# Performance work log

Hardware: AMD Instinct MI355X
Metric: run time of the kernel (lower is better)

The kernel has to match this reference:

```python
import jax, jax.numpy as jnp
import numpy as np

EPS = 1e-8


def setup_inputs() -> dict:
    key = jax.random.key(0)
    ks = jax.random.split(key, 10)
    B, Cin, H, W = 16, 256, 64, 64
    D, C = 128, 32
    return {
        "f_curr": jax.random.normal(ks[0], (B, Cin, H, W), jnp.float32),
        "mu_prior": jax.random.normal(ks[1], (B, D, C), jnp.float32),
        "log_sigma_prior": jax.random.normal(ks[2], (B, D, C), jnp.float32),
        "pi_prior": jax.random.uniform(ks[3], (B, C), jnp.float32),
        "mu_post": jax.random.normal(ks[4], (B, D), jnp.float32),
        "log_sigma_post": jax.random.normal(ks[5], (B, D), jnp.float32),
        "noise_cluster": jax.random.normal(ks[6], (B, D), jnp.float32),
        "noise_z": jax.random.normal(ks[7], (B, D), jnp.float32),
        "proj_W": jax.random.normal(ks[8], (Cin, Cin + D), jnp.float32) * 0.02,
        "proj_b": jax.random.normal(ks[9], (Cin,), jnp.float32) * 0.02,
    }


def reference(f_curr, mu_prior, log_sigma_prior, pi_prior, mu_post,
              log_sigma_post, noise_cluster, noise_z, proj_W, proj_b):
    sg = jax.lax.stop_gradient

    # ---- _cluster_sampler (all stats detached in the original) ----
    mu_p, ls_p = sg(mu_post), sg(log_sigma_post)          # [B, D]
    mu_pr, ls_pr = sg(mu_prior), sg(log_sigma_prior)      # [B, D, C]
    z_post = mu_p + jnp.exp(ls_p) * noise_cluster          # Normal(mu, exp(ls)).sample()
    sigma_pr = jnp.exp(ls_pr)
    # Normal log_prob of z_post[:, :, None] under each cluster -> [B, D, C]
    log_probs = (-ls_pr - 0.5 * jnp.log(2.0 * jnp.pi)
                 - (z_post[:, :, None] - mu_pr) ** 2 / (2.0 * sigma_pr ** 2))
    log_prob_c = jnp.sum(log_probs, axis=1)                # [B, C]
    pi_post = jax.nn.softmax(log_prob_c, axis=1)           # [B, C]

    # ---- z_c = Normal(mu_post, exp(ls)+eps).sample()  (no grad: .sample()) ----
    z_c = sg(mu_post + (jnp.exp(log_sigma_post) + EPS) * noise_z)  # [B, D]

    # ---- _f_combine: concat + 1x1 conv, computed as split matmuls ----
    Cin = f_curr.shape[1]
    Wf, Wz = proj_W[:, :Cin], proj_W[:, Cin:]              # [Cin,Cin], [Cin,D]
    bias = jnp.einsum('bd,od->bo', z_c, Wz) + proj_b       # spatially-constant part
    f_out = jnp.einsum('bchw,oc->bohw', f_curr, Wf) + bias[:, :, None, None]

    # ---- _kld ----
    mu_post_e = mu_post[:, :, None]                        # [B, D, 1]
    ls_post_e = log_sigma_post[:, :, None]
    sigma_prior = jnp.exp(log_sigma_prior)
    sigma_post = jnp.exp(ls_post_e)
    kl_g = (log_sigma_prior - ls_post_e
            + (sigma_post ** 2 + (mu_post_e - mu_prior) ** 2)
            / (2.0 * sigma_prior ** 2 + EPS) - 0.5)
    kl_g = jnp.sum(kl_g, axis=1)                           # [B, C]
    kl_g_weighted = jnp.sum(pi_post * kl_g, axis=1)        # [B]
    kl_cat = jnp.sum(pi_post * (jnp.log(pi_post + EPS) - jnp.log(pi_prior + EPS)), axis=1)  # [B]
    kl_std = jnp.sum(-ls_post_e + 0.5 * (jnp.exp(2.0 * ls_post_e) + mu_post_e ** 2) - 0.5,
                     axis=1)                               # [B, 1]
    # NOTE: original torch code broadcasts [B] + [B,1] -> [B,B] before mean; replicated here.
    kld = jnp.mean((kl_g_weighted + kl_cat) + kl_std)

    return f_out, kld
```

## Files before the change

### kernel.cpp

```cpp
#include <hip/hip_runtime.h>
#include <math.h>

#define EPS_F 1e-8f

typedef __attribute__((ext_vector_type(8))) short bf16x8;
typedef __attribute__((ext_vector_type(4))) float f32x4;

__device__ inline short f2bf(float f) {
    union { float f; unsigned u; } v; v.f = f;
    unsigned r = (v.u + 0x7fffu + ((v.u >> 16) & 1u)) >> 16;
    return (short)r;
}

__global__ __launch_bounds__(256) void prelim_kernel(
    const float* __restrict__ mu_prior,
    const float* __restrict__ ls_prior,
    const float* __restrict__ pi_prior,
    const float* __restrict__ mu_post,
    const float* __restrict__ ls_post,
    const float* __restrict__ noise_c,
    const float* __restrict__ noise_z,
    const float* __restrict__ projW,
    const float* __restrict__ projb,
    float* __restrict__ ws_bias,
    short* __restrict__ ws_A,
    float* __restrict__ kld_out)
{
    const int b = blockIdx.x;
    const int t = threadIdx.x;

    {
        const float* wrow = projW + t * 384 + b * 16;
        bf16x8 w0, w1;
#pragma unroll
        for (int j = 0; j < 8; ++j) w0[j] = f2bf(wrow[j]);
#pragma unroll
        for (int j = 0; j < 8; ++j) w1[j] = f2bf(wrow[8 + j]);
        *(bf16x8*)&ws_A[(b * 2 + 0) * 2048 + t * 8] = w0;
        *(bf16x8*)&ws_A[(b * 2 + 1) * 2048 + t * 8] = w1;
    }

    __shared__ float s_zpost[128];
    __shared__ float s_zc[128];
    __shared__ float s_mu[128];
    __shared__ float s_e2[128];
    __shared__ float s_lsp[128];
    __shared__ float s_kstd[128];
    __shared__ float s_p1[8][32];
    __shared__ float s_p2[8][32];

    if (t < 128) {
        const float mu = mu_post[b * 128 + t];
        const float ls = ls_post[b * 128 + t];
        const float el = __expf(ls);
        s_zpost[t] = mu + el * noise_c[b * 128 + t];
        s_zc[t]    = mu + (el + EPS_F) * noise_z[b * 128 + t];
        s_mu[t]    = mu;
        s_e2[t]    = el * el;
        s_lsp[t]   = ls;
        s_kstd[t]  = -ls + 0.5f * (el * el + mu * mu) - 0.5f;
    }
    __syncthreads();

    {
        const int c = t & 31;
        const int g = t >> 5;
        const float* mpB = mu_prior + b * 4096;
        const float* lpB = ls_prior + b * 4096;
        float lp = 0.f, kg = 0.f;
#pragma unroll 4
        for (int j = 0; j < 16; ++j) {
            const int d = g * 16 + j;
            const float mpr  = mpB[d * 32 + c];
            const float lpr  = lpB[d * 32 + c];
            const float inv2 = 0.5f * __expf(-2.f * lpr);
            const float zd   = s_zpost[d] - mpr;
            lp += -lpr - 0.91893853320467274f - zd * zd * inv2;
            const float dm   = s_mu[d] - mpr;
            const float e2pr = __expf(2.f * lpr);
            kg += lpr - s_lsp[d]
                + (s_e2[d] + dm * dm) * __builtin_amdgcn_rcpf(2.f * e2pr + EPS_F)
                - 0.5f;
        }
        s_p1[g][c] = lp;
        s_p2[g][c] = kg;
    }
    __syncthreads();

    if (t < 64) {
        const int c = t & 31;
        float lp = 0.f, kg = 0.f;
#pragma unroll
        for (int g = 0; g < 8; ++g) { lp += s_p1[g][c]; kg += s_p2[g][c]; }
        float ks = s_kstd[c] + s_kstd[c + 32] + s_kstd[c + 64] + s_kstd[c + 96];
        const float pp = pi_prior[b * 32 + c];

        float m = lp;
#pragma unroll
        for (int o = 16; o; o >>= 1) m = fmaxf(m, __shfl_xor(m, o, 32));
        const float e = __expf(lp - m);
        float den = e;
#pragma unroll
        for (int o = 16; o; o >>= 1) den += __shfl_xor(den, o, 32);
        const float pi = e * __builtin_amdgcn_rcpf(den);
        float tot = pi * kg + pi * (__logf(pi + EPS_F) - __logf(pp + EPS_F));
#pragma unroll
        for (int o = 16; o; o >>= 1) tot += __shfl_xor(tot, o, 32);
#pragma unroll
        for (int o = 16; o; o >>= 1) ks += __shfl_xor(ks, o, 32);
        if (t == 0) atomicAdd(kld_out, (tot + ks) * 0.0625f);
    }

    {
        const int o = t;
        const float4* wrow = (const float4*)(projW + o * 384 + 256);
        float sum = projb[o];
#pragma unroll 8
        for (int j = 0; j < 32; ++j) {
            const float4 w = wrow[j];
            sum += s_zc[4 * j + 0] * w.x + s_zc[4 * j + 1] * w.y +
                   s_zc[4 * j + 2] * w.z + s_zc[4 * j + 3] * w.w;
        }
        ws_bias[b * 256 + o] = sum;
    }
}

__global__ __launch_bounds__(256) void gemm_kernel(
    const float* __restrict__ F,
    const short* __restrict__ wsA,
    const float* __restrict__ bias,
    float* __restrict__ O)
{
    const int nT = blockIdx.x;
    const int b  = blockIdx.y;

    __shared__ short Bl[32][64][8];
    __shared__ float s_bias[256];

    const int tid  = threadIdx.x;
    const int lane = tid & 63;
    const int wave = tid >> 6;
    const int kg   = lane >> 4;
    const int lm   = lane & 15;

    s_bias[tid] = bias[b * 256 + tid];

    const int sn4 = (tid & 15) * 4;
    const int skb = (tid >> 4) * 16;
    const float* fp = F + (size_t)b * 1048576 + (size_t)skb * 4096
                    + nT * 64 + sn4;

    float4 ld[16];
#pragma unroll
    for (int i = 0; i < 16; ++i)
        ld[i] = *(const float4*)(fp + (size_t)i * 4096);

#pragma unroll
    for (int h = 0; h < 2; ++h) {
        const int kgi = (skb >> 3) + h;
#pragma unroll
        for (int c = 0; c < 4; ++c) {
            bf16x8 v;
#pragma unroll
            for (int j = 0; j < 8; ++j) {
                const float4 q = ld[h * 8 + j];
                v[j] = f2bf(c == 0 ? q.x : c == 1 ? q.y : c == 2 ? q.z : q.w);
            }
            *(bf16x8*)&Bl[kgi][sn4 + c][0] = v;
        }
    }
    __syncthreads();

    const short* aBase = wsA + (size_t)kg * 2048 + (wave * 64 + lm) * 8;

    f32x4 acc[4][4];
#pragma unroll
    for (int i = 0; i < 4; ++i)
#pragma unroll
        for (int j = 0; j < 4; ++j) acc[i][j] = (f32x4){0.f, 0.f, 0.f, 0.f};

#pragma unroll
    for (int kc = 0; kc < 8; ++kc) {
        bf16x8 aF[4], bF[4];
#pragma unroll
        for (int mt = 0; mt < 4; ++mt)
            aF[mt] = *(const bf16x8*)(aBase + (size_t)kc * 8192 + mt * 128);
#pragma unroll
        for (int nt = 0; nt < 4; ++nt)
            bF[nt] = *(const bf16x8*)&Bl[kc * 4 + kg][nt * 16 + lm][0];

#pragma unroll
        for (int mt = 0; mt < 4; ++mt)
#pragma unroll
            for (int nt = 0; nt < 4; ++nt)
                acc[mt][nt] = __builtin_amdgcn_mfma_f32_16x16x32_bf16(
                    aF[mt], bF[nt], acc[mt][nt], 0, 0, 0);
    }

    float* Ob = O + (size_t)b * 1048576 + nT * 64;
    const int rbase = wave * 64 + kg * 4;
    const int cbase = lm;
#pragma unroll
    for (int mt = 0; mt < 4; ++mt) {
#pragma unroll
        for (int r = 0; r < 4; ++r) {
            const int row = rbase + mt * 16 + r;
            const float bb = s_bias[row];
            float* orow = Ob + (size_t)row * 4096 + cbase;
#pragma unroll
            for (int nt = 0; nt < 4; ++nt)
                orow[nt * 16] = acc[mt][nt][r] + bb;
        }
    }
}

extern "C" void kernel_launch(void* const* d_in, const int* in_sizes, int n_in,
                              void* d_out, int out_size, void* d_ws, size_t ws_size,
                              hipStream_t stream) {
    const float* f_curr   = (const float*)d_in[0];
    const float* mu_prior = (const float*)d_in[1];
    const float* ls_prior = (const float*)d_in[2];
    const float* pi_prior = (const float*)d_in[3];
    const float* mu_post  = (const float*)d_in[4];
    const float* ls_post  = (const float*)d_in[5];
    const float* noise_c  = (const float*)d_in[6];
    const float* noise_z  = (const float*)d_in[7];
    const float* projW    = (const float*)d_in[8];
    const float* projb    = (const float*)d_in[9];

    float* out = (float*)d_out;
    float* ws  = (float*)d_ws;
    float* ws_bias = ws;
    short* ws_A    = (short*)(ws + 4096);

    float* kld_out = out + 16777216;
    hipMemsetAsync(kld_out, 0, sizeof(float), stream);

    prelim_kernel<<<16, 256, 0, stream>>>(mu_prior, ls_prior, pi_prior, mu_post,
                                          ls_post, noise_c, noise_z, projW, projb,
                                          ws_bias, ws_A, kld_out);
    gemm_kernel<<<dim3(64, 16), 256, 0, stream>>>(f_curr, ws_A, ws_bias, out);
}
```

Baseline: 146.1 us.

## Split setup into parallel blocks, swizzle LDS, vectorize output stores, drop memset

The preliminary kernel's three jobs (weight bf16 conversion, KL statistics, bias projection) now run in 48 independent blocks instead of 16 serialized ones. Per-batch KL partials go to workspace and are summed by one GEMM thread, which removes the memset and the atomic. The GEMM XOR-swizzles its LDS tile to avoid bank conflicts and swaps the MFMA operands so each lane holds four consecutive columns, allowing float4 output stores. It also uses hardware bf16 conversion and adds a launch_bounds occupancy hint.

```diff
diff --git a/kernel.cpp b/kernel.cpp
--- a/kernel.cpp
+++ b/kernel.cpp
@@ -7,12 +7,14 @@
 typedef __attribute__((ext_vector_type(4))) float f32x4;
 
 __device__ inline short f2bf(float f) {
-    union { float f; unsigned u; } v; v.f = f;
-    unsigned r = (v.u + 0x7fffu + ((v.u >> 16) & 1u)) >> 16;
-    return (short)r;
-}
-
-__global__ __launch_bounds__(256) void prelim_kernel(
+    return (short)__builtin_bit_cast(unsigned short, (__bf16)f);
+}
+
+__device__ inline int bswz(int kgi, int n) {
+    return (kgi * 512 + n * 8) ^ (((n >> 3) & 3) << 4);
+}
+
+__global__ __launch_bounds__(256) void setup_kernel(
     const float* __restrict__ mu_prior,
     const float* __restrict__ ls_prior,
     const float* __restrict__ pi_prior,
@@ -24,21 +26,10 @@
     const float* __restrict__ projb,
     float* __restrict__ ws_bias,
     short* __restrict__ ws_A,
-    float* __restrict__ kld_out)
+    float* __restrict__ ws_kld)
 {
-    const int b = blockIdx.x;
+    const int g = blockIdx.x;
     const int t = threadIdx.x;
-
-    {
-        const float* wrow = projW + t * 384 + b * 16;
-        bf16x8 w0, w1;
-#pragma unroll
-        for (int j = 0; j < 8; ++j) w0[j] = f2bf(wrow[j]);
-#pragma unroll
-        for (int j = 0; j < 8; ++j) w1[j] = f2bf(wrow[8 + j]);
-        *(bf16x8*)&ws_A[(b * 2 + 0) * 2048 + t * 8] = w0;
-        *(bf16x8*)&ws_A[(b * 2 + 1) * 2048 + t * 8] = w1;
-    }
 
     __shared__ float s_zpost[128];
     __shared__ float s_zc[128];
@@ -49,92 +40,115 @@
     __shared__ float s_p1[8][32];
     __shared__ float s_p2[8][32];
 
-    if (t < 128) {
-        const float mu = mu_post[b * 128 + t];
-        const float ls = ls_post[b * 128 + t];
-        const float el = __expf(ls);
-        s_zpost[t] = mu + el * noise_c[b * 128 + t];
-        s_zc[t]    = mu + (el + EPS_F) * noise_z[b * 128 + t];
-        s_mu[t]    = mu;
-        s_e2[t]    = el * el;
-        s_lsp[t]   = ls;
-        s_kstd[t]  = -ls + 0.5f * (el * el + mu * mu) - 0.5f;
-    }
-    __syncthreads();
+    if (g < 16) {
+        const float* wrow = projW + t * 384 + g * 16;
+        bf16x8 w0, w1;
+#pragma unroll
+        for (int j = 0; j < 8; ++j) w0[j] = f2bf(wrow[j]);
+#pragma unroll
+        for (int j = 0; j < 8; ++j) w1[j] = f2bf(wrow[8 + j]);
+        *(bf16x8*)&ws_A[(g * 2 + 0) * 2048 + t * 8] = w0;
+        *(bf16x8*)&ws_A[(g * 2 + 1) * 2048 + t * 8] = w1;
+        return;
+    }
+
+    if (g < 32) {
+        const int b = g - 16;
+        if (t < 128) {
+            const float mu = mu_post[b * 128 + t];
+            const float ls = ls_post[b * 128 + t];
+            const float el = __expf(ls);
+            s_zpost[t] = mu + el * noise_c[b * 128 + t];
+            s_mu[t]    = mu;
+            s_e2[t]    = el * el;
+            s_lsp[t]   = ls;
+            s_kstd[t]  = -ls + 0.5f * (el * el + mu * mu) - 0.5f;
+        }
+        __syncthreads();
+
+        {
+            const int c  = t & 31;
+            const int gg = t >> 5;
+            const float* mpB = mu_prior + b * 4096;
+            const float* lpB = ls_prior + b * 4096;
+            float lp = 0.f, kgv = 0.f;
+#pragma unroll 4
+            for (int j = 0; j < 16; ++j) {
+                const int d = gg * 16 + j;
+                const float mpr  = mpB[d * 32 + c];
+                const float lpr  = lpB[d * 32 + c];
+                const float inv2 = 0.5f * __expf(-2.f * lpr);
+                const float zd   = s_zpost[d] - mpr;
+                lp += -lpr - 0.91893853320467274f - zd * zd * inv2;
+                const float dm   = s_mu[d] - mpr;
+                const float e2pr = __expf(2.f * lpr);
+                kgv += lpr - s_lsp[d]
+                     + (s_e2[d] + dm * dm) * __builtin_amdgcn_rcpf(2.f * e2pr + EPS_F)
+                     - 0.5f;
+            }
+            s_p1[gg][c] = lp;
+            s_p2[gg][c] = kgv;
+        }
+        __syncthreads();
+
+        if (t < 64) {
+            const int c = t & 31;
+            float lp = 0.f, kgv = 0.f;
+#pragma unroll
+            for (int gg = 0; gg < 8; ++gg) { lp += s_p1[gg][c]; kgv += s_p2[gg][c]; }
+            float ks = s_kstd[c] + s_kstd[c + 32] + s_kstd[c + 64] + s_kstd[c + 96];
+            const float pp = pi_prior[b * 32 + c];
+
+            float m = lp;
+#pragma unroll
+            for (int o = 16; o; o >>= 1) m = fmaxf(m, __shfl_xor(m, o, 32));
+            const float e = __expf(lp - m);
+            float den = e;
+#pragma unroll
+            for (int o = 16; o; o >>= 1) den += __shfl_xor(den, o, 32);
+            const float pi = e * __builtin_amdgcn_rcpf(den);
+            float tot = pi * kgv + pi * (__logf(pi + EPS_F) - __logf(pp + EPS_F));
+#pragma unroll
+            for (int o = 16; o; o >>= 1) tot += __shfl_xor(tot, o, 32);
+#pragma unroll
+            for (int o = 16; o; o >>= 1) ks += __shfl_xor(ks, o, 32);
+            if (t == 0) ws_kld[b] = tot + ks;
+        }
+        return;
+    }
 
     {
-        const int c = t & 31;
-        const int g = t >> 5;
-        const float* mpB = mu_prior + b * 4096;
-        const float* lpB = ls_prior + b * 4096;
-        float lp = 0.f, kg = 0.f;
-#pragma unroll 4
-        for (int j = 0; j < 16; ++j) {
-            const int d = g * 16 + j;
-            const float mpr  = mpB[d * 32 + c];
-            const float lpr  = lpB[d * 32 + c];
-            const float inv2 = 0.5f * __expf(-2.f * lpr);
-            const float zd   = s_zpost[d] - mpr;
-            lp += -lpr - 0.91893853320467274f - zd * zd * inv2;
-            const float dm   = s_mu[d] - mpr;
-            const float e2pr = __expf(2.f * lpr);
-            kg += lpr - s_lsp[d]
-                + (s_e2[d] + dm * dm) * __builtin_amdgcn_rcpf(2.f * e2pr + EPS_F)
-                - 0.5f;
-        }
-        s_p1[g][c] = lp;
-        s_p2[g][c] = kg;
-    }
-    __syncthreads();
-
-    if (t < 64) {
-        const int c = t & 31;
-        float lp = 0.f, kg = 0.f;
-#pragma unroll
-        for (int g = 0; g < 8; ++g) { lp += s_p1[g][c]; kg += s_p2[g][c]; }
-        float ks = s_kstd[c] + s_kstd[c + 32] + s_kstd[c + 64] + s_kstd[c + 96];
-        const float pp = pi_prior[b * 32 + c];
-
-        float m = lp;
-#pragma unroll
-        for (int o = 16; o; o >>= 1) m = fmaxf(m, __shfl_xor(m, o, 32));
-        const float e = __expf(lp - m);
-        float den = e;
-#pragma unroll
-        for (int o = 16; o; o >>= 1) den += __shfl_xor(den, o, 32);
-        const float pi = e * __builtin_amdgcn_rcpf(den);
-        float tot = pi * kg + pi * (__logf(pi + EPS_F) - __logf(pp + EPS_F));
-#pragma unroll
-        for (int o = 16; o; o >>= 1) tot += __shfl_xor(tot, o, 32);
-#pragma unroll
-        for (int o = 16; o; o >>= 1) ks += __shfl_xor(ks, o, 32);
-        if (t == 0) atomicAdd(kld_out, (tot + ks) * 0.0625f);
-    }
-
-    {
-        const int o = t;
-        const float4* wrow = (const float4*)(projW + o * 384 + 256);
-        float sum = projb[o];
+        const int b = g - 32;
+        if (t < 128) {
+            const float mu = mu_post[b * 128 + t];
+            const float el = __expf(ls_post[b * 128 + t]);
+            s_zc[t] = mu + (el + EPS_F) * noise_z[b * 128 + t];
+        }
+        __syncthreads();
+
+        const float4* wrow = (const float4*)(projW + t * 384 + 256);
+        float sum = projb[t];
 #pragma unroll 8
         for (int j = 0; j < 32; ++j) {
             const float4 w = wrow[j];
             sum += s_zc[4 * j + 0] * w.x + s_zc[4 * j + 1] * w.y +
                    s_zc[4 * j + 2] * w.z + s_zc[4 * j + 3] * w.w;
         }
-        ws_bias[b * 256 + o] = sum;
-    }
-}
-
-__global__ __launch_bounds__(256) void gemm_kernel(
+        ws_bias[b * 256 + t] = sum;
+    }
+}
+
+__global__ __launch_bounds__(256, 4) void gemm_kernel(
     const float* __restrict__ F,
     const short* __restrict__ wsA,
     const float* __restrict__ bias,
+    const float* __restrict__ ws_kld,
     float* __restrict__ O)
 {
     const int nT = blockIdx.x;
     const int b  = blockIdx.y;
 
-    __shared__ short Bl[32][64][8];
+    __shared__ short Bl[32 * 64 * 8];
     __shared__ float s_bias[256];
 
     const int tid  = threadIdx.x;
@@ -145,6 +159,13 @@
 
     s_bias[tid] = bias[b * 256 + tid];
 
+    if (nT == 0 && b == 0 && tid == 0) {
+        float s = 0.f;
+#pragma unroll
+        for (int i = 0; i < 16; ++i) s += ws_kld[i];
+        O[16777216] = s * 0.0625f;
+    }
+
     const int sn4 = (tid & 15) * 4;
     const int skb = (tid >> 4) * 16;
     const float* fp = F + (size_t)b * 1048576 + (size_t)skb * 4096
@@ -166,7 +187,7 @@
                 const float4 q = ld[h * 8 + j];
                 v[j] = f2bf(c == 0 ? q.x : c == 1 ? q.y : c == 2 ? q.z : q.w);
             }
-            *(bf16x8*)&Bl[kgi][sn4 + c][0] = v;
+            *(bf16x8*)&Bl[bswz(kgi, sn4 + c)] = v;
         }
     }
     __syncthreads();
@@ -181,35 +202,36 @@
 
 #pragma unroll
     for (int kc = 0; kc < 8; ++kc) {
-        bf16x8 aF[4], bF[4];
+        bf16x8 aW[4], bF[4];
 #pragma unroll
         for (int mt = 0; mt < 4; ++mt)
-            aF[mt] = *(const bf16x8*)(aBase + (size_t)kc * 8192 + mt * 128);
+            aW[mt] = *(const bf16x8*)(aBase + (size_t)kc * 8192 + mt * 128);
 #pragma unroll
         for (int nt = 0; nt < 4; ++nt)
-            bF[nt] = *(const bf16x8*)&Bl[kc * 4 + kg][nt * 16 + lm][0];
+            bF[nt] = *(const bf16x8*)&Bl[bswz(kc * 4 + kg, nt * 16 + lm)];
 
 #pragma unroll
         for (int mt = 0; mt < 4; ++mt)
 #pragma unroll
             for (int nt = 0; nt < 4; ++nt)
                 acc[mt][nt] = __builtin_amdgcn_mfma_f32_16x16x32_bf16(
-                    aF[mt], bF[nt], acc[mt][nt], 0, 0, 0);
-    }
-
-    float* Ob = O + (size_t)b * 1048576 + nT * 64;
-    const int rbase = wave * 64 + kg * 4;
-    const int cbase = lm;
+                    bF[nt], aW[mt], acc[mt][nt], 0, 0, 0);
+    }
+
+    float* Ob = O + (size_t)b * 1048576 + nT * 64 + kg * 4;
 #pragma unroll
     for (int mt = 0; mt < 4; ++mt) {
-#pragma unroll
-        for (int r = 0; r < 4; ++r) {
-            const int row = rbase + mt * 16 + r;
-            const float bb = s_bias[row];
-            float* orow = Ob + (size_t)row * 4096 + cbase;
-#pragma unroll
-            for (int nt = 0; nt < 4; ++nt)
-                orow[nt * 16] = acc[mt][nt][r] + bb;
+        const int m = wave * 64 + mt * 16 + lm;
+        const float bb = s_bias[m];
+        float* orow = Ob + (size_t)m * 4096;
+#pragma unroll
+        for (int nt = 0; nt < 4; ++nt) {
+            float4 o4;
+            o4.x = acc[mt][nt][0] + bb;
+            o4.y = acc[mt][nt][1] + bb;
+            o4.z = acc[mt][nt][2] + bb;
+            o4.w = acc[mt][nt][3] + bb;
+            *(float4*)(orow + nt * 16) = o4;
         }
     }
 }
@@ -232,12 +254,10 @@
     float* ws  = (float*)d_ws;
     float* ws_bias = ws;
     short* ws_A    = (short*)(ws + 4096);
-
-    float* kld_out = out + 16777216;
-    hipMemsetAsync(kld_out, 0, sizeof(float), stream);
-
-    prelim_kernel<<<16, 256, 0, stream>>>(mu_prior, ls_prior, pi_prior, mu_post,
-                                          ls_post, noise_c, noise_z, projW, projb,
-                                          ws_bias, ws_A, kld_out);
-    gemm_kernel<<<dim3(64, 16), 256, 0, stream>>>(f_curr, ws_A, ws_bias, out);
-}
+    float* ws_kld  = ws + 4096 + 32768;
+
+    setup_kernel<<<48, 256, 0, stream>>>(mu_prior, ls_prior, pi_prior, mu_post,
+                                         ls_post, noise_c, noise_z, projW, projb,
+                                         ws_bias, ws_A, ws_kld);
+    gemm_kernel<<<dim3(64, 16), 256, 0, stream>>>(f_curr, ws_A, ws_bias, ws_kld, out);
+}
```

Result: faster. 136.2 us (-6.8%).
